# Optimization experiments

Measured on AMD Instinct MI355X. Metric: run time of the kernel, lower is better.

## Reference

```python
import jax, jax.numpy as jnp
import numpy as np

N_NODES = 10000
N_EDGES = 160000
HIDDEN = 64
NUM_RBF = 32
Q_DIM = 8
CUTOFF_UPPER = 5.0


def silu(x):
    return x * jax.nn.sigmoid(x)


def tensor_norm(X):
    # X: [n, 3, 3, H] -> [n, H] (Frobenius norm squared over the 3x3 dims)
    return (X * X).sum(axis=(1, 2))


def decompose_tensor(X):
    # X: [n, 3, 3, H] -> I: [n, H] (trace/3), A: antisym [n,3,3,H], S: sym traceless [n,3,3,H]
    eye = jnp.eye(3, dtype=X.dtype)[None, :, :, None]
    I = jnp.einsum('naah->nh', X) / 3.0
    Xt = X.transpose(0, 2, 1, 3)
    A = 0.5 * (X - Xt)
    S = 0.5 * (X + Xt) - I[:, None, None, :] * eye
    return I, A, S


def compose_tensor(I, A, S):
    eye = jnp.eye(3, dtype=A.dtype)[None, :, :, None]
    return I[:, None, None, :] * eye + A + S


def tmm(P, Q):
    # 3x3 matmul per (atom, channel): [n,3,3,H] x [n,3,3,H] -> [n,3,3,H]
    return jnp.einsum('nach,ncbh->nabh', P, Q)


def setup_inputs() -> dict:
    key = jax.random.key(0)
    ks = jax.random.split(key, 16)
    H = HIDDEN
    inp = {
        'X': jax.random.normal(ks[0], (N_NODES, 3, 3, H), jnp.float32),
        'charges': jax.random.normal(ks[1], (N_NODES, Q_DIM), jnp.float32),
        'edge_weight': jax.random.uniform(ks[2], (N_EDGES,), jnp.float32) * CUTOFF_UPPER,
        'edge_attr': jax.random.normal(ks[3], (N_EDGES, NUM_RBF), jnp.float32),
        'edge_index': jax.random.randint(ks[4], (2, N_EDGES), 0, N_NODES, jnp.int32),
    }
    d_in = NUM_RBF + 2 * Q_DIM
    inp['Ws1'] = jax.random.normal(ks[5], (d_in, H), jnp.float32) / np.sqrt(d_in).astype(np.float32)
    inp['bs1'] = jnp.zeros((H,), jnp.float32)
    inp['Ws2'] = jax.random.normal(ks[6], (H, 2 * H), jnp.float32) / np.sqrt(H).astype(np.float32)
    inp['bs2'] = jnp.zeros((2 * H,), jnp.float32)
    inp['Ws3'] = jax.random.normal(ks[7], (2 * H, 3 * H), jnp.float32) / np.sqrt(2 * H).astype(np.float32)
    inp['bs3'] = jnp.zeros((3 * H,), jnp.float32)
    for i in range(6):
        inp['Wt%d' % i] = jax.random.normal(ks[8 + i], (H, H), jnp.float32) / np.sqrt(H).astype(np.float32)
    return inp


def reference(X, charges, edge_weight, edge_attr, Ws1, bs1, Ws2, bs2, Ws3, bs3,
              Wt0, Wt1, Wt2, Wt3, Wt4, Wt5, edge_index):
    H = HIDDEN
    n = X.shape[0]
    row, col = edge_index[0], edge_index[1]
    # cosine cutoff (cutoff_lower = 0)
    C = 0.5 * (jnp.cos(edge_weight * (jnp.pi / CUTOFF_UPPER)) + 1.0)
    C = C * (edge_weight < CUTOFF_UPPER).astype(X.dtype)
    # edge scalar MLP on [rbf, q_i, q_j]
    h = jnp.concatenate([edge_attr, charges[row], charges[col]], axis=-1)
    h = silu(h @ Ws1 + bs1)
    h = silu(h @ Ws2 + bs2)
    h = silu(h @ Ws3 + bs3)
    w = (h * C[:, None]).reshape(h.shape[0], 3, H)  # [E, 3, H]
    # normalize node tensors
    X = X / (tensor_norm(X) + 1.0)[:, None, None, :]
    I, A, S = decompose_tensor(X)
    I = I @ Wt0
    A = A @ Wt1
    S = S @ Wt2
    Y = compose_tensor(I, A, S)
    # message passing: gather I/A/S at source (edge_index[1]), weight per component, scatter-add at dest (edge_index[0])
    eye = jnp.eye(3, dtype=X.dtype)[None, :, :, None]
    msg_e = ((w[:, 0] * I[col])[:, None, None, :] * eye
             + w[:, 1][:, None, None, :] * A[col]
             + w[:, 2][:, None, None, :] * S[col])  # [E, 3, 3, H]
    msg = jax.ops.segment_sum(msg_e, row, num_segments=n)  # [n, 3, 3, H]
    # O(3): C = msg @ Y + Y @ msg (3x3 matmul per channel)
    Cm = tmm(msg, Y) + tmm(Y, msg)
    I2, A2, S2 = decompose_tensor(Cm)
    normp1 = tensor_norm(Cm) + 1.0
    I2 = I2 / normp1
    A2 = A2 / normp1[:, None, None, :]
    S2 = S2 / normp1[:, None, None, :]
    I2 = I2 @ Wt3
    A2 = A2 @ Wt4
    S2 = S2 @ Wt5
    dX = compose_tensor(I2, A2, S2)
    return X + dX + tmm(dX, dX)
```

## Files before the change

### kernel.cpp

```cpp
#include <hip/hip_runtime.h>
#include <math.h>

#define HD 64

typedef _Float16 half8 __attribute__((ext_vector_type(8)));
typedef _Float16 half4v __attribute__((ext_vector_type(4)));
typedef float floatx4 __attribute__((ext_vector_type(4)));

__device__ __forceinline__ float silu_f(float x) {
    return x * __builtin_amdgcn_rcpf(1.0f + __expf(-x));
}

__global__ __launch_bounds__(256) void pre_wconv_count(
    const float* __restrict__ X,
    const float* __restrict__ Wt0, const float* __restrict__ Wt1, const float* __restrict__ Wt2,
    float* __restrict__ Tn, _Float16* __restrict__ TnH, int N, int nbPre,
    const float* __restrict__ Ws1, const float* __restrict__ Ws2, const float* __restrict__ Ws3,
    _Float16* __restrict__ W1f, _Float16* __restrict__ W2f, _Float16* __restrict__ W3f,
    const int* __restrict__ edge_index, int* __restrict__ cnt, int E)
{
    if (blockIdx.x >= nbPre + 144) {
        int e = (blockIdx.x - nbPre - 144) * 256 + threadIdx.x;
        if (e < E) atomicAdd(&cnt[edge_index[e]], 1);
        return;
    }
    if (blockIdx.x >= nbPre) {
        int id = (blockIdx.x - nbPre) * 256 + threadIdx.x;
        if (id < 4096) {
            int i = id & 7, l = (id >> 3) & 63, t = id >> 9;
            int s = t >> 2, nt = t & 3;
            int k = s * 32 + (l >> 4) * 8 + i;
            int n = nt * 16 + (l & 15);
            W1f[id] = (k < 48) ? (_Float16)Ws1[k * 64 + n] : (_Float16)0.f;
        } else if (id < 4096 + 8192) {
            int j = id - 4096;
            int i = j & 7, l = (j >> 3) & 63, t = j >> 9;
            int s = t >> 3, nt = t & 7;
            int k = s * 32 + (l >> 4) * 8 + i;
            int n = nt * 16 + (l & 15);
            W2f[j] = (_Float16)Ws2[k * 128 + n];
        } else if (id < 4096 + 8192 + 24576) {
            int j = id - 4096 - 8192;
            int i = j & 7, l = (j >> 3) & 63, t = j >> 9;
            int s = t / 12, nt = t % 12;
            int k = s * 32 + (l >> 4) * 8 + i;
            int n = nt * 16 + (l & 15);
            W3f[j] = (_Float16)Ws3[k * 192 + n];
        }
        return;
    }

    int sub = threadIdx.x >> 6;
    int h = threadIdx.x & 63;
    int n = blockIdx.x * 4 + sub;
    int nn = (n < N) ? n : (N - 1);

    const float* Xb = X + (size_t)nn * 9 * HD + h;
    float x[9];
    float nrm = 0.f;
#pragma unroll
    for (int i = 0; i < 9; ++i) { x[i] = Xb[i * HD]; nrm += x[i] * x[i]; }
    float inv = 1.0f / (nrm + 1.0f);
#pragma unroll
    for (int i = 0; i < 9; ++i) x[i] *= inv;

    float I0 = (x[0] + x[4] + x[8]) * (1.0f / 3.0f);
    __shared__ float comp[4][10][HD];
    comp[sub][0][h] = I0;
    comp[sub][1][h] = 0.5f * (x[1] - x[3]);
    comp[sub][2][h] = 0.5f * (x[2] - x[6]);
    comp[sub][3][h] = 0.5f * (x[5] - x[7]);
    comp[sub][4][h] = x[0] - I0;
    comp[sub][5][h] = 0.5f * (x[1] + x[3]);
    comp[sub][6][h] = 0.5f * (x[2] + x[6]);
    comp[sub][7][h] = x[4] - I0;
    comp[sub][8][h] = 0.5f * (x[5] + x[7]);
    comp[sub][9][h] = x[8] - I0;
    __syncthreads();
    float acc[10];
#pragma unroll
    for (int i = 0; i < 10; ++i) acc[i] = 0.f;
    for (int k = 0; k < HD; ++k) {
        float w0 = Wt0[k * HD + h];
        float w1 = Wt1[k * HD + h];
        float w2 = Wt2[k * HD + h];
        acc[0] += comp[sub][0][k] * w0;
        acc[1] += comp[sub][1][k] * w1;
        acc[2] += comp[sub][2][k] * w1;
        acc[3] += comp[sub][3][k] * w1;
#pragma unroll
        for (int j = 0; j < 6; ++j) acc[4 + j] += comp[sub][4 + j][k] * w2;
    }
    if (n < N) {
        float* tp = Tn + (size_t)n * 640 + h;
        _Float16* th = TnH + (size_t)n * 640 + h;
#pragma unroll
        for (int i = 0; i < 10; ++i) {
            tp[i * 64] = acc[i];
            th[i * 64] = (_Float16)acc[i];
        }
    }
}

__global__ __launch_bounds__(1024) void scan_kernel(
    const int* __restrict__ cnt, int* __restrict__ offs, int* __restrict__ curs, int N)
{
    __shared__ int partials[16];
    __shared__ int base_s;
    int tid = threadIdx.x, wid = tid >> 6, lane = tid & 63;
    if (tid == 0) base_s = 0;
    __syncthreads();
    for (int start = 0; start < N; start += 1024) {
        int i = start + tid;
        int v = (i < N) ? cnt[i] : 0;
        int s = v;
#pragma unroll
        for (int d = 1; d < 64; d <<= 1) {
            int t = __shfl_up(s, d, 64);
            if (lane >= d) s += t;
        }
        if (lane == 63) partials[wid] = s;
        __syncthreads();
        if (tid == 0) {
            int run = base_s;
#pragma unroll
            for (int w = 0; w < 16; ++w) { int t = partials[w]; partials[w] = run; run += t; }
            base_s = run;
        }
        __syncthreads();
        int excl = partials[wid] + s - v;
        if (i < N) { offs[i] = excl; curs[i] = excl; }
        __syncthreads();
    }
    if (tid == 0) offs[N] = base_s;
}

__global__ __launch_bounds__(256, 5) void mlp_mfma(
    const float* __restrict__ edge_attr, const float* __restrict__ charges,
    const float* __restrict__ edge_weight, const int* __restrict__ edge_index,
    int* __restrict__ curs, int* __restrict__ colP,
    const _Float16* __restrict__ W1f, const float* __restrict__ bs1,
    const _Float16* __restrict__ W2f, const float* __restrict__ bs2,
    const _Float16* __restrict__ W3f, const float* __restrict__ bs3,
    _Float16* __restrict__ bufH, int E)
{
    __shared__ __align__(16) _Float16 act[64][200];
    __shared__ float cvsS[64];
    __shared__ int rankSS[64];

    int tid = threadIdx.x;
    int wv = tid >> 6, l = tid & 63;
    int base = blockIdx.x * 64;
    int row16 = l & 15, quad = l >> 4;

#pragma unroll
    for (int i = 0; i < 4; ++i) {
        int slot = tid + i * 256;
        int e_l = slot >> 4, f = slot & 15;
        int e = base + e_l;
        int ee = (e < E) ? e : (E - 1);
        float4 v = make_float4(0.f, 0.f, 0.f, 0.f);
        if (f < 8) {
            v = *(const float4*)(edge_attr + (size_t)ee * 32 + f * 4);
        } else if (f < 10) {
            int r = edge_index[ee];
            v = *(const float4*)(charges + (size_t)r * 8 + (f - 8) * 4);
        } else if (f < 12) {
            int c = edge_index[E + ee];
            v = *(const float4*)(charges + (size_t)c * 8 + (f - 10) * 4);
        }
        half4v hv = { (_Float16)v.x, (_Float16)v.y, (_Float16)v.z, (_Float16)v.w };
        *(half4v*)&act[e_l][f * 4] = hv;
    }
    if (tid < 64) {
        int e = base + tid;
        bool valid = (e < E);
        int ee = valid ? e : (E - 1);
        int row = edge_index[ee];
        int col = edge_index[E + ee];
        int rk = 0;
        if (valid) {
            rk = atomicAdd(&curs[row], 1);
            colP[rk] = col;
        }
        rankSS[tid] = rk;
        float wgt = edge_weight[ee];
        float cv = 0.5f * (__cosf(wgt * 0.6283185307179586f) + 1.0f);
        cvsS[tid] = (wgt < 5.0f) ? cv : 0.0f;
    }
    __syncthreads();

    {
        half8 w0 = *(const half8*)(W1f + ((size_t)(0 * 4 + wv) * 64 + l) * 8);
        half8 w1 = *(const half8*)(W1f + ((size_t)(1 * 4 + wv) * 64 + l) * 8);
        floatx4 acc1[4];
#pragma unroll
        for (int m = 0; m < 4; ++m) {
            floatx4 c = {0.f, 0.f, 0.f, 0.f};
            c = __builtin_amdgcn_mfma_f32_16x16x32_f16(
                    *(const half8*)&act[m * 16 + row16][quad * 8], w0, c, 0, 0, 0);
            c = __builtin_amdgcn_mfma_f32_16x16x32_f16(
                    *(const half8*)&act[m * 16 + row16][32 + quad * 8], w1, c, 0, 0, 0);
            acc1[m] = c;
        }
        float b = bs1[wv * 16 + row16];
#pragma unroll
        for (int m = 0; m < 4; ++m)
#pragma unroll
            for (int r = 0; r < 4; ++r)
                act[m * 16 + quad * 4 + r][128 + wv * 16 + row16] =
                    (_Float16)silu_f(acc1[m][r] + b);
    }
    __syncthreads();

    {
        floatx4 acc2[4][2];
#pragma unroll
        for (int m = 0; m < 4; ++m)
#pragma unroll
            for (int j = 0; j < 2; ++j) acc2[m][j] = (floatx4){0.f, 0.f, 0.f, 0.f};
#pragma unroll
        for (int s = 0; s < 2; ++s) {
            half8 w0 = *(const half8*)(W2f + ((size_t)(s * 8 + wv * 2 + 0) * 64 + l) * 8);
            half8 w1 = *(const half8*)(W2f + ((size_t)(s * 8 + wv * 2 + 1) * 64 + l) * 8);
#pragma unroll
            for (int m = 0; m < 4; ++m) {
                half8 a = *(const half8*)&act[m * 16 + row16][128 + s * 32 + quad * 8];
                acc2[m][0] = __builtin_amdgcn_mfma_f32_16x16x32_f16(a, w0, acc2[m][0], 0, 0, 0);
                acc2[m][1] = __builtin_amdgcn_mfma_f32_16x16x32_f16(a, w1, acc2[m][1], 0, 0, 0);
            }
        }
        float b0 = bs2[(wv * 2 + 0) * 16 + row16];
        float b1 = bs2[(wv * 2 + 1) * 16 + row16];
#pragma unroll
        for (int m = 0; m < 4; ++m)
#pragma unroll
            for (int r = 0; r < 4; ++r) {
                act[m * 16 + quad * 4 + r][(wv * 2 + 0) * 16 + row16] =
                    (_Float16)silu_f(acc2[m][0][r] + b0);
                act[m * 16 + quad * 4 + r][(wv * 2 + 1) * 16 + row16] =
                    (_Float16)silu_f(acc2[m][1][r] + b1);
            }
    }
    __syncthreads();

    floatx4 acc3[4][3];
#pragma unroll
    for (int m = 0; m < 4; ++m)
#pragma unroll
        for (int j = 0; j < 3; ++j) acc3[m][j] = (floatx4){0.f, 0.f, 0.f, 0.f};
#pragma unroll
    for (int s = 0; s < 4; ++s) {
        half8 w0 = *(const half8*)(W3f + ((size_t)(s * 12 + wv * 3 + 0) * 64 + l) * 8);
        half8 w1 = *(const half8*)(W3f + ((size_t)(s * 12 + wv * 3 + 1) * 64 + l) * 8);
        half8 w2 = *(const half8*)(W3f + ((size_t)(s * 12 + wv * 3 + 2) * 64 + l) * 8);
#pragma unroll
        for (int m = 0; m < 4; ++m) {
            half8 a = *(const half8*)&act[m * 16 + row16][s * 32 + quad * 8];
            acc3[m][0] = __builtin_amdgcn_mfma_f32_16x16x32_f16(a, w0, acc3[m][0], 0, 0, 0);
            acc3[m][1] = __builtin_amdgcn_mfma_f32_16x16x32_f16(a, w1, acc3[m][1], 0, 0, 0);
            acc3[m][2] = __builtin_amdgcn_mfma_f32_16x16x32_f16(a, w2, acc3[m][2], 0, 0, 0);
        }
    }
    __syncthreads();

    {
        float b0 = bs3[(wv * 3 + 0) * 16 + row16];
        float b1 = bs3[(wv * 3 + 1) * 16 + row16];
        float b2 = bs3[(wv * 3 + 2) * 16 + row16];
#pragma unroll
        for (int m = 0; m < 4; ++m) {
#pragma unroll
            for (int r = 0; r < 4; ++r) {
                float cv = cvsS[m * 16 + quad * 4 + r];
                act[m * 16 + quad * 4 + r][(wv * 3 + 0) * 16 + row16] =
                    (_Float16)(silu_f(acc3[m][0][r] + b0) * cv);
                act[m * 16 + quad * 4 + r][(wv * 3 + 1) * 16 + row16] =
                    (_Float16)(silu_f(acc3[m][1][r] + b1) * cv);
                act[m * 16 + quad * 4 + r][(wv * 3 + 2) * 16 + row16] =
                    (_Float16)(silu_f(acc3[m][2][r] + b2) * cv);
            }
        }
    }
    __syncthreads();

    {
        int fr = tid >> 2;
        int ef = base + fr;
        if (ef < E) {
            _Float16* dst = bufH + (size_t)rankSS[fr] * 192;
#pragma unroll
            for (int i = 0; i < 6; ++i) {
                int j = (tid & 3) + i * 4;
                *(half8*)(dst + j * 8) = *(const half8*)&act[fr][j * 8];
            }
        }
    }
}

__global__ __launch_bounds__(256) void msg_kernel(
    const _Float16* __restrict__ bufH, const int* __restrict__ colP,
    const int* __restrict__ offs, const _Float16* __restrict__ TnH,
    float* __restrict__ Mn, int N)
{
    __shared__ float part[4][10][64];
    int qtr = threadIdx.x >> 6;
    int lane = threadIdx.x & 63;
    int n = blockIdx.x;
    int beg = offs[n], end = offs[n + 1];
    int len = end - beg;
    int s0 = beg + (len * qtr) / 4;
    int s1 = beg + (len * (qtr + 1)) / 4;

    float a0 = 0.f, a1 = 0.f, a2 = 0.f, a3 = 0.f, a4 = 0.f;
    float a5 = 0.f, a6 = 0.f, a7 = 0.f, a8 = 0.f, a9 = 0.f;
#pragma unroll 2
    for (int idx = s0; idx < s1; ++idx) {
        int c = colP[idx];
        const _Float16* wp = bufH + (size_t)idx * 192;
        float w0 = (float)wp[lane];
        float w1 = (float)wp[64 + lane];
        float w2 = (float)wp[128 + lane];
        const _Float16* tp = TnH + (size_t)c * 640;
        a0 += w0 * (float)tp[lane];
        a1 += w1 * (float)tp[64 + lane];
        a2 += w1 * (float)tp[128 + lane];
        a3 += w1 * (float)tp[192 + lane];
        a4 += w2 * (float)tp[256 + lane];
        a5 += w2 * (float)tp[320 + lane];
        a6 += w2 * (float)tp[384 + lane];
        a7 += w2 * (float)tp[448 + lane];
        a8 += w2 * (float)tp[512 + lane];
        a9 += w2 * (float)tp[576 + lane];
    }
    part[qtr][0][lane] = a0; part[qtr][1][lane] = a1;
    part[qtr][2][lane] = a2; part[qtr][3][lane] = a3;
    part[qtr][4][lane] = a4; part[qtr][5][lane] = a5;
    part[qtr][6][lane] = a6; part[qtr][7][lane] = a7;
    part[qtr][8][lane] = a8; part[qtr][9][lane] = a9;
    __syncthreads();

    if (qtr < 2) {
        float* mp = Mn + (size_t)n * 640;
#pragma unroll
        for (int j = 0; j < 5; ++j) {
            int c = qtr * 5 + j;
            mp[c * 64 + lane] = (part[0][c][lane] + part[1][c][lane])
                              + (part[2][c][lane] + part[3][c][lane]);
        }
    }
}

__global__ __launch_bounds__(256) void node_post(
    const float* __restrict__ X,
    const float* __restrict__ Tn, const float* __restrict__ Mn,
    const float* __restrict__ Wt3, const float* __restrict__ Wt4, const float* __restrict__ Wt5,
    float* __restrict__ out, int N)
{
    int sub = threadIdx.x >> 6;
    int h = threadIdx.x & 63;
    int n = blockIdx.x * 4 + sub;
    int nn = (n < N) ? n : (N - 1);

    const float* Xb = X + (size_t)nn * 9 * HD + h;
    float x[9];
    float nr = 0.f;
#pragma unroll
    for (int i = 0; i < 9; ++i) { x[i] = Xb[i * HD]; nr += x[i] * x[i]; }
    float xinv = 1.0f / (nr + 1.0f);
#pragma unroll
    for (int i = 0; i < 9; ++i) x[i] *= xinv;

    const float* tp = Tn + (size_t)nn * 640 + h;
    const float* mp = Mn + (size_t)nn * 640 + h;
    float yI = tp[0], mI = mp[0];
    float yA[3], yS[6], mA[3], mS[6];
#pragma unroll
    for (int j = 0; j < 3; ++j) { yA[j] = tp[(1 + j) * 64]; mA[j] = mp[(1 + j) * 64]; }
#pragma unroll
    for (int j = 0; j < 6; ++j) { yS[j] = tp[(4 + j) * 64]; mS[j] = mp[(4 + j) * 64]; }

    float M[3][3] = {
        { mI + mS[0],     mA[0] + mS[1],   mA[1] + mS[2] },
        { -mA[0] + mS[1], mI + mS[3],      mA[2] + mS[4] },
        { -mA[1] + mS[2], -mA[2] + mS[4],  mI + mS[5] } };
    float Y[3][3] = {
        { yI + yS[0],     yA[0] + yS[1],   yA[1] + yS[2] },
        { -yA[0] + yS[1], yI + yS[3],      yA[2] + yS[4] },
        { -yA[1] + yS[2], -yA[2] + yS[4],  yI + yS[5] } };

    float Cm[3][3];
    float nrm = 0.f;
#pragma unroll
    for (int a = 0; a < 3; ++a) {
#pragma unroll
        for (int b = 0; b < 3; ++b) {
            float s = 0.f;
#pragma unroll
            for (int c = 0; c < 3; ++c) s += M[a][c] * Y[c][b] + Y[a][c] * M[c][b];
            Cm[a][b] = s;
            nrm += s * s;
        }
    }
    float inv = 1.0f / (nrm + 1.0f);
    float tr3 = (Cm[0][0] + Cm[1][1] + Cm[2][2]) * (1.0f / 3.0f);

    __shared__ float comp[4][10][HD];
    comp[sub][0][h] = tr3 * inv;
    comp[sub][1][h] = 0.5f * (Cm[0][1] - Cm[1][0]) * inv;
    comp[sub][2][h] = 0.5f * (Cm[0][2] - Cm[2][0]) * inv;
    comp[sub][3][h] = 0.5f * (Cm[1][2] - Cm[2][1]) * inv;
    comp[sub][4][h] = (Cm[0][0] - tr3) * inv;
    comp[sub][5][h] = 0.5f * (Cm[0][1] + Cm[1][0]) * inv;
    comp[sub][6][h] = 0.5f * (Cm[0][2] + Cm[2][0]) * inv;
    comp[sub][7][h] = (Cm[1][1] - tr3) * inv;
    comp[sub][8][h] = 0.5f * (Cm[1][2] + Cm[2][1]) * inv;
    comp[sub][9][h] = (Cm[2][2] - tr3) * inv;
    __syncthreads();

    float acc[10];
#pragma unroll
    for (int i = 0; i < 10; ++i) acc[i] = 0.f;
    for (int k = 0; k < HD; ++k) {
        float w3 = Wt3[k * HD + h];
        float w4 = Wt4[k * HD + h];
        float w5 = Wt5[k * HD + h];
        acc[0] += comp[sub][0][k] * w3;
        acc[1] += comp[sub][1][k] * w4;
        acc[2] += comp[sub][2][k] * w4;
        acc[3] += comp[sub][3][k] * w4;
#pragma unroll
        for (int j = 0; j < 6; ++j) acc[4 + j] += comp[sub][4 + j][k] * w5;
    }
    float D[3][3] = {
        { acc[0] + acc[4],  acc[1] + acc[5],  acc[2] + acc[6] },
        { -acc[1] + acc[5], acc[0] + acc[7],  acc[3] + acc[8] },
        { -acc[2] + acc[6], -acc[3] + acc[8], acc[0] + acc[9] } };

    if (n < N) {
        float* ob = out + (size_t)n * 9 * HD + h;
#pragma unroll
        for (int a = 0; a < 3; ++a) {
#pragma unroll
            for (int b = 0; b < 3; ++b) {
                float s = 0.f;
#pragma unroll
                for (int c = 0; c < 3; ++c) s += D[a][c] * D[c][b];
                ob[(a * 3 + b) * HD] = x[a * 3 + b] + D[a][b] + s;
            }
        }
    }
}

extern "C" void kernel_launch(void* const* d_in, const int* in_sizes, int n_in,
                              void* d_out, int out_size, void* d_ws, size_t ws_size,
                              hipStream_t stream)
{
    const float* X           = (const float*)d_in[0];
    const float* charges     = (const float*)d_in[1];
    const float* edge_weight = (const float*)d_in[2];
    const float* edge_attr   = (const float*)d_in[3];
    const int*   edge_index  = (const int*)d_in[4];
    const float* Ws1 = (const float*)d_in[5];
    const float* bs1 = (const float*)d_in[6];
    const float* Ws2 = (const float*)d_in[7];
    const float* bs2 = (const float*)d_in[8];
    const float* Ws3 = (const float*)d_in[9];
    const float* bs3 = (const float*)d_in[10];
    const float* Wt0 = (const float*)d_in[11];
    const float* Wt1 = (const float*)d_in[12];
    const float* Wt2 = (const float*)d_in[13];
    const float* Wt3 = (const float*)d_in[14];
    const float* Wt4 = (const float*)d_in[15];
    const float* Wt5 = (const float*)d_in[16];

    int N = in_sizes[0] / (9 * HD);
    int E = in_sizes[2];

    float* ws = (float*)d_ws;
    float* Tn  = ws;
    float* Mn  = Tn + (size_t)N * 640;
    _Float16* TnH  = (_Float16*)(Mn + (size_t)N * 640);
    _Float16* bufH = TnH + (size_t)N * 640;
    int* cnt   = (int*)(bufH + (size_t)E * 192);
    int* offs  = cnt + N;
    int* curs  = offs + N + 1;
    int* colP  = curs + N;
    size_t fofs = ((size_t)((char*)(colP + E) - (char*)d_ws) + 15) & ~(size_t)15;
    _Float16* W1f = (_Float16*)((char*)d_ws + fofs);
    _Float16* W2f = W1f + 4096;
    _Float16* W3f = W2f + 8192;

    hipMemsetAsync(cnt, 0, (size_t)N * sizeof(int), stream);

    int nbPre = (N + 3) / 4;
    int nbE256 = (E + 255) / 256;
    pre_wconv_count<<<nbPre + 144 + nbE256, 256, 0, stream>>>(
        X, Wt0, Wt1, Wt2, Tn, TnH, N, nbPre,
        Ws1, Ws2, Ws3, W1f, W2f, W3f, edge_index, cnt, E);

    scan_kernel<<<1, 1024, 0, stream>>>(cnt, offs, curs, N);

    int nbE64 = (E + 63) / 64;
    mlp_mfma<<<nbE64, 256, 0, stream>>>(edge_attr, charges, edge_weight, edge_index,
                                        curs, colP, W1f, bs1, W2f, bs2, W3f, bs3, bufH, E);

    msg_kernel<<<N, 256, 0, stream>>>(bufH, colP, offs, TnH, Mn, N);

    node_post<<<(N + 3) / 4, 256, 0, stream>>>(X, Tn, Mn, Wt3, Wt4, Wt5, (float*)d_out, N);
}
```

Baseline: 159.3 us.

## Process 128 edges per MLP block and store message sums in half precision

The edge MLP kernel now handles 128 edges per block instead of 64. Layer-3 weights are held in registers and reused across two 64-edge halves, and the first half's activation writeback overlaps the second half's MFMAs. The intent is to amortize weight loads and barriers over more edges and halve the number of blocks, at the cost of more LDS and registers, which lowers occupancy to 4 blocks per SIMD. Separately, the per-node message sums are written as fp16 instead of fp32, which halves that traffic but adds rounding error.

New measurement: 176.2 us. 10.6% more time.

```diff
diff --git a/kernel.cpp b/kernel.cpp
--- a/kernel.cpp
+++ b/kernel.cpp
@@ -135,7 +135,7 @@
     if (tid == 0) offs[N] = base_s;
 }
 
-__global__ __launch_bounds__(256, 5) void mlp_mfma(
+__global__ __launch_bounds__(256, 4) void mlp_mfma(
     const float* __restrict__ edge_attr, const float* __restrict__ charges,
     const float* __restrict__ edge_weight, const int* __restrict__ edge_index,
     int* __restrict__ curs, int* __restrict__ colP,
@@ -144,17 +144,17 @@
     const _Float16* __restrict__ W3f, const float* __restrict__ bs3,
     _Float16* __restrict__ bufH, int E)
 {
-    __shared__ __align__(16) _Float16 act[64][200];
-    __shared__ float cvsS[64];
-    __shared__ int rankSS[64];
+    __shared__ __align__(16) _Float16 act[128][200];
+    __shared__ float cvsS[128];
+    __shared__ int rankSS[128];
 
     int tid = threadIdx.x;
     int wv = tid >> 6, l = tid & 63;
-    int base = blockIdx.x * 64;
+    int base = blockIdx.x * 128;
     int row16 = l & 15, quad = l >> 4;
 
 #pragma unroll
-    for (int i = 0; i < 4; ++i) {
+    for (int i = 0; i < 8; ++i) {
         int slot = tid + i * 256;
         int e_l = slot >> 4, f = slot & 15;
         int e = base + e_l;
@@ -172,7 +172,7 @@
         half4v hv = { (_Float16)v.x, (_Float16)v.y, (_Float16)v.z, (_Float16)v.w };
         *(half4v*)&act[e_l][f * 4] = hv;
     }
-    if (tid < 64) {
+    if (tid < 128) {
         int e = base + tid;
         bool valid = (e < E);
         int ee = valid ? e : (E - 1);
@@ -193,9 +193,9 @@
     {
         half8 w0 = *(const half8*)(W1f + ((size_t)(0 * 4 + wv) * 64 + l) * 8);
         half8 w1 = *(const half8*)(W1f + ((size_t)(1 * 4 + wv) * 64 + l) * 8);
-        floatx4 acc1[4];
-#pragma unroll
-        for (int m = 0; m < 4; ++m) {
+        floatx4 acc1[8];
+#pragma unroll
+        for (int m = 0; m < 8; ++m) {
             floatx4 c = {0.f, 0.f, 0.f, 0.f};
             c = __builtin_amdgcn_mfma_f32_16x16x32_f16(
                     *(const half8*)&act[m * 16 + row16][quad * 8], w0, c, 0, 0, 0);
@@ -205,7 +205,7 @@
         }
         float b = bs1[wv * 16 + row16];
 #pragma unroll
-        for (int m = 0; m < 4; ++m)
+        for (int m = 0; m < 8; ++m)
 #pragma unroll
             for (int r = 0; r < 4; ++r)
                 act[m * 16 + quad * 4 + r][128 + wv * 16 + row16] =
@@ -214,9 +214,9 @@
     __syncthreads();
 
     {
-        floatx4 acc2[4][2];
-#pragma unroll
-        for (int m = 0; m < 4; ++m)
+        floatx4 acc2[8][2];
+#pragma unroll
+        for (int m = 0; m < 8; ++m)
 #pragma unroll
             for (int j = 0; j < 2; ++j) acc2[m][j] = (floatx4){0.f, 0.f, 0.f, 0.f};
 #pragma unroll
@@ -224,7 +224,7 @@
             half8 w0 = *(const half8*)(W2f + ((size_t)(s * 8 + wv * 2 + 0) * 64 + l) * 8);
             half8 w1 = *(const half8*)(W2f + ((size_t)(s * 8 + wv * 2 + 1) * 64 + l) * 8);
 #pragma unroll
-            for (int m = 0; m < 4; ++m) {
+            for (int m = 0; m < 8; ++m) {
                 half8 a = *(const half8*)&act[m * 16 + row16][128 + s * 32 + quad * 8];
                 acc2[m][0] = __builtin_amdgcn_mfma_f32_16x16x32_f16(a, w0, acc2[m][0], 0, 0, 0);
                 acc2[m][1] = __builtin_amdgcn_mfma_f32_16x16x32_f16(a, w1, acc2[m][1], 0, 0, 0);
@@ -233,7 +233,7 @@
         float b0 = bs2[(wv * 2 + 0) * 16 + row16];
         float b1 = bs2[(wv * 2 + 1) * 16 + row16];
 #pragma unroll
-        for (int m = 0; m < 4; ++m)
+        for (int m = 0; m < 8; ++m)
 #pragma unroll
             for (int r = 0; r < 4; ++r) {
                 act[m * 16 + quad * 4 + r][(wv * 2 + 0) * 16 + row16] =
@@ -244,44 +244,60 @@
     }
     __syncthreads();
 
-    floatx4 acc3[4][3];
+    half8 w3[12];
+#pragma unroll
+    for (int s = 0; s < 4; ++s)
+#pragma unroll
+        for (int j = 0; j < 3; ++j)
+            w3[s * 3 + j] = *(const half8*)(W3f + ((size_t)(s * 12 + wv * 3 + j) * 64 + l) * 8);
+
+    float b0 = bs3[(wv * 3 + 0) * 16 + row16];
+    float b1 = bs3[(wv * 3 + 1) * 16 + row16];
+    float b2 = bs3[(wv * 3 + 2) * 16 + row16];
+
+    floatx4 accA[4][3];
 #pragma unroll
     for (int m = 0; m < 4; ++m)
 #pragma unroll
-        for (int j = 0; j < 3; ++j) acc3[m][j] = (floatx4){0.f, 0.f, 0.f, 0.f};
-#pragma unroll
-    for (int s = 0; s < 4; ++s) {
-        half8 w0 = *(const half8*)(W3f + ((size_t)(s * 12 + wv * 3 + 0) * 64 + l) * 8);
-        half8 w1 = *(const half8*)(W3f + ((size_t)(s * 12 + wv * 3 + 1) * 64 + l) * 8);
-        half8 w2 = *(const half8*)(W3f + ((size_t)(s * 12 + wv * 3 + 2) * 64 + l) * 8);
+        for (int j = 0; j < 3; ++j) accA[m][j] = (floatx4){0.f, 0.f, 0.f, 0.f};
+#pragma unroll
+    for (int s = 0; s < 4; ++s)
 #pragma unroll
         for (int m = 0; m < 4; ++m) {
             half8 a = *(const half8*)&act[m * 16 + row16][s * 32 + quad * 8];
-            acc3[m][0] = __builtin_amdgcn_mfma_f32_16x16x32_f16(a, w0, acc3[m][0], 0, 0, 0);
-            acc3[m][1] = __builtin_amdgcn_mfma_f32_16x16x32_f16(a, w1, acc3[m][1], 0, 0, 0);
-            acc3[m][2] = __builtin_amdgcn_mfma_f32_16x16x32_f16(a, w2, acc3[m][2], 0, 0, 0);
-        }
-    }
-    __syncthreads();
-
-    {
-        float b0 = bs3[(wv * 3 + 0) * 16 + row16];
-        float b1 = bs3[(wv * 3 + 1) * 16 + row16];
-        float b2 = bs3[(wv * 3 + 2) * 16 + row16];
+            accA[m][0] = __builtin_amdgcn_mfma_f32_16x16x32_f16(a, w3[s * 3 + 0], accA[m][0], 0, 0, 0);
+            accA[m][1] = __builtin_amdgcn_mfma_f32_16x16x32_f16(a, w3[s * 3 + 1], accA[m][1], 0, 0, 0);
+            accA[m][2] = __builtin_amdgcn_mfma_f32_16x16x32_f16(a, w3[s * 3 + 2], accA[m][2], 0, 0, 0);
+        }
+    __syncthreads();
+
+#pragma unroll
+    for (int m = 0; m < 4; ++m) {
+#pragma unroll
+        for (int r = 0; r < 4; ++r) {
+            float cv = cvsS[m * 16 + quad * 4 + r];
+            act[m * 16 + quad * 4 + r][(wv * 3 + 0) * 16 + row16] =
+                (_Float16)(silu_f(accA[m][0][r] + b0) * cv);
+            act[m * 16 + quad * 4 + r][(wv * 3 + 1) * 16 + row16] =
+                (_Float16)(silu_f(accA[m][1][r] + b1) * cv);
+            act[m * 16 + quad * 4 + r][(wv * 3 + 2) * 16 + row16] =
+                (_Float16)(silu_f(accA[m][2][r] + b2) * cv);
+        }
+    }
+    floatx4 accB[4][3];
+#pragma unroll
+    for (int m = 0; m < 4; ++m)
+#pragma unroll
+        for (int j = 0; j < 3; ++j) accB[m][j] = (floatx4){0.f, 0.f, 0.f, 0.f};
+#pragma unroll
+    for (int s = 0; s < 4; ++s)
 #pragma unroll
         for (int m = 0; m < 4; ++m) {
-#pragma unroll
-            for (int r = 0; r < 4; ++r) {
-                float cv = cvsS[m * 16 + quad * 4 + r];
-                act[m * 16 + quad * 4 + r][(wv * 3 + 0) * 16 + row16] =
-                    (_Float16)(silu_f(acc3[m][0][r] + b0) * cv);
-                act[m * 16 + quad * 4 + r][(wv * 3 + 1) * 16 + row16] =
-                    (_Float16)(silu_f(acc3[m][1][r] + b1) * cv);
-                act[m * 16 + quad * 4 + r][(wv * 3 + 2) * 16 + row16] =
-                    (_Float16)(silu_f(acc3[m][2][r] + b2) * cv);
-            }
-        }
-    }
+            half8 a = *(const half8*)&act[64 + m * 16 + row16][s * 32 + quad * 8];
+            accB[m][0] = __builtin_amdgcn_mfma_f32_16x16x32_f16(a, w3[s * 3 + 0], accB[m][0], 0, 0, 0);
+            accB[m][1] = __builtin_amdgcn_mfma_f32_16x16x32_f16(a, w3[s * 3 + 1], accB[m][1], 0, 0, 0);
+            accB[m][2] = __builtin_amdgcn_mfma_f32_16x16x32_f16(a, w3[s * 3 + 2], accB[m][2], 0, 0, 0);
+        }
     __syncthreads();
 
     {
@@ -296,12 +312,39 @@
             }
         }
     }
+#pragma unroll
+    for (int m = 0; m < 4; ++m) {
+#pragma unroll
+        for (int r = 0; r < 4; ++r) {
+            float cv = cvsS[64 + m * 16 + quad * 4 + r];
+            act[64 + m * 16 + quad * 4 + r][(wv * 3 + 0) * 16 + row16] =
+                (_Float16)(silu_f(accB[m][0][r] + b0) * cv);
+            act[64 + m * 16 + quad * 4 + r][(wv * 3 + 1) * 16 + row16] =
+                (_Float16)(silu_f(accB[m][1][r] + b1) * cv);
+            act[64 + m * 16 + quad * 4 + r][(wv * 3 + 2) * 16 + row16] =
+                (_Float16)(silu_f(accB[m][2][r] + b2) * cv);
+        }
+    }
+    __syncthreads();
+
+    {
+        int fr = 64 + (tid >> 2);
+        int ef = base + fr;
+        if (ef < E) {
+            _Float16* dst = bufH + (size_t)rankSS[fr] * 192;
+#pragma unroll
+            for (int i = 0; i < 6; ++i) {
+                int j = (tid & 3) + i * 4;
+                *(half8*)(dst + j * 8) = *(const half8*)&act[fr][j * 8];
+            }
+        }
+    }
 }
 
 __global__ __launch_bounds__(256) void msg_kernel(
     const _Float16* __restrict__ bufH, const int* __restrict__ colP,
     const int* __restrict__ offs, const _Float16* __restrict__ TnH,
-    float* __restrict__ Mn, int N)
+    _Float16* __restrict__ MnH, int N)
 {
     __shared__ float part[4][10][64];
     int qtr = threadIdx.x >> 6;
@@ -341,19 +384,19 @@
     __syncthreads();
 
     if (qtr < 2) {
-        float* mp = Mn + (size_t)n * 640;
+        _Float16* mp = MnH + (size_t)n * 640;
 #pragma unroll
         for (int j = 0; j < 5; ++j) {
             int c = qtr * 5 + j;
-            mp[c * 64 + lane] = (part[0][c][lane] + part[1][c][lane])
-                              + (part[2][c][lane] + part[3][c][lane]);
+            mp[c * 64 + lane] = (_Float16)((part[0][c][lane] + part[1][c][lane])
+                                         + (part[2][c][lane] + part[3][c][lane]));
         }
     }
 }
 
 __global__ __launch_bounds__(256) void node_post(
     const float* __restrict__ X,
-    const float* __restrict__ Tn, const float* __restrict__ Mn,
+    const float* __restrict__ Tn, const _Float16* __restrict__ MnH,
     const float* __restrict__ Wt3, const float* __restrict__ Wt4, const float* __restrict__ Wt5,
     float* __restrict__ out, int N)
 {
@@ -372,13 +415,13 @@
     for (int i = 0; i < 9; ++i) x[i] *= xinv;
 
     const float* tp = Tn + (size_t)nn * 640 + h;
-    const float* mp = Mn + (size_t)nn * 640 + h;
-    float yI = tp[0], mI = mp[0];
+    const _Float16* mp = MnH + (size_t)nn * 640 + h;
+    float yI = tp[0], mI = (float)mp[0];
     float yA[3], yS[6], mA[3], mS[6];
 #pragma unroll
-    for (int j = 0; j < 3; ++j) { yA[j] = tp[(1 + j) * 64]; mA[j] = mp[(1 + j) * 64]; }
-#pragma unroll
-    for (int j = 0; j < 6; ++j) { yS[j] = tp[(4 + j) * 64]; mS[j] = mp[(4 + j) * 64]; }
+    for (int j = 0; j < 3; ++j) { yA[j] = tp[(1 + j) * 64]; mA[j] = (float)mp[(1 + j) * 64]; }
+#pragma unroll
+    for (int j = 0; j < 6; ++j) { yS[j] = tp[(4 + j) * 64]; mS[j] = (float)mp[(4 + j) * 64]; }
 
     float M[3][3] = {
         { mI + mS[0],     mA[0] + mS[1],   mA[1] + mS[2] },
@@ -479,9 +522,9 @@
 
     float* ws = (float*)d_ws;
     float* Tn  = ws;
-    float* Mn  = Tn + (size_t)N * 640;
-    _Float16* TnH  = (_Float16*)(Mn + (size_t)N * 640);
-    _Float16* bufH = TnH + (size_t)N * 640;
+    _Float16* TnH  = (_Float16*)(Tn + (size_t)N * 640);
+    _Float16* MnH  = TnH + (size_t)N * 640;
+    _Float16* bufH = MnH + (size_t)N * 640;
     int* cnt   = (int*)(bufH + (size_t)E * 192);
     int* offs  = cnt + N;
     int* curs  = offs + N + 1;
@@ -501,11 +544,11 @@
 
     scan_kernel<<<1, 1024, 0, stream>>>(cnt, offs, curs, N);
 
-    int nbE64 = (E + 63) / 64;
-    mlp_mfma<<<nbE64, 256, 0, stream>>>(edge_attr, charges, edge_weight, edge_index,
-                                        curs, colP, W1f, bs1, W2f, bs2, W3f, bs3, bufH, E);
-
-    msg_kernel<<<N, 256, 0, stream>>>(bufH, colP, offs, TnH, Mn, N);
-
-    node_post<<<(N + 3) / 4, 256, 0, stream>>>(X, Tn, Mn, Wt3, Wt4, Wt5, (float*)d_out, N);
-}
+    int nbE128 = (E + 127) / 128;
+    mlp_mfma<<<nbE128, 256, 0, stream>>>(edge_attr, charges, edge_weight, edge_index,
+                                         curs, colP, W1f, bs1, W2f, bs2, W3f, bs3, bufH, E);
+
+    msg_kernel<<<N, 256, 0, stream>>>(bufH, colP, offs, TnH, MnH, N);
+
+    node_post<<<(N + 3) / 4, 256, 0, stream>>>(X, Tn, MnH, Wt3, Wt4, Wt5, (float*)d_out, N);
+}
```
